# Performance work log

Measured on AMD Instinct MI355X. Metric: run time of the kernel, lower is better.

## Reference

```python
import jax, jax.numpy as jnp
import numpy as np

BITS = 4
GROUP = 128
MAXQ = 2 ** BITS - 1  # 15 for asymmetric 4-bit


def round_ste(x):
    # straight-through rounding: round in fwd, identity in bwd
    return x + jax.lax.stop_gradient(jnp.round(x) - x)


def quant_weight(weight, v, min_scale, max_scale):
    """Groupwise asymmetric fake-quant (quantize + dequantize) of weight.

    weight: [O, I], v: [O, I] learnable rounding offsets,
    min_scale/max_scale: [O*I/GROUP] learnable min/max scales in [-1, 0].
    """
    O, I = weight.shape
    w = weight.reshape(-1, GROUP)          # [G, GROUP]
    vv = v.reshape(-1, GROUP)              # [G, GROUP]
    wmin_t = jnp.minimum(w.min(axis=1), 0.0)  # [G]
    wmax_t = jnp.maximum(w.max(axis=1), 0.0)  # [G]
    # forward clamps min/max scale into [-1, 0] before use
    wmin = wmin_t * (jnp.clip(min_scale, -1.0, 0.0) + 1.0)
    wmax = wmax_t * (jnp.clip(max_scale, -1.0, 0.0) + 1.0)
    degenerate = (wmin == 0.0) & (wmax == 0.0)
    wmin = jnp.where(degenerate, -1.0, wmin)
    wmax = jnp.where(degenerate, 1.0, wmax)
    # scale stored at fp16 precision (scale_dtype), then used in fp32 math
    scale = ((wmax - wmin) / MAXQ).astype(jnp.float16).astype(weight.dtype)  # [G]
    zp = round_ste(-wmin / scale)                                            # [G]
    int_w = round_ste(w / scale[:, None] + vv)                               # [G, GROUP]
    q = jnp.clip(int_w + zp[:, None], 0.0, float(MAXQ))
    wq = scale[:, None] * (q - zp[:, None])
    return wq.reshape(O, I)


def setup_inputs() -> dict:
    key = jax.random.key(0)
    k_x, k_w, k_b, k_v = jax.random.split(key, 4)
    O, I = 4096, 4096
    B, S = 2, 2048
    x = jax.random.normal(k_x, (B, S, I), dtype=jnp.float32)
    weight = jax.random.normal(k_w, (O, I), dtype=jnp.float32) * 0.02
    bias = jax.random.normal(k_b, (O,), dtype=jnp.float32) * 0.02
    value = jax.random.normal(k_v, (O, I), dtype=jnp.float32) * 0.1
    n_groups = O * I // GROUP
    min_scale = jnp.zeros((n_groups,), dtype=jnp.float32)
    max_scale = jnp.zeros((n_groups,), dtype=jnp.float32)
    return {"x": x, "weight": weight, "bias": bias, "value": value,
            "min_scale": min_scale, "max_scale": max_scale}


def reference(x, weight, bias, value, min_scale, max_scale):
    wq = quant_weight(weight, value, min_scale, max_scale)  # [O, I]
    # F.linear(x, weight_q, bias): x @ wq.T + bias
    return jnp.einsum('bsi,oi->bso', x, wq) + bias
```

## Files before the change

### kernel.cpp

```cpp
#include <hip/hip_runtime.h>
#include <hip/hip_bf16.h>
#include <hip/hip_fp16.h>
#include <stdint.h>

#define M_DIM 4096
#define N_DIM 4096
#define K_DIM 4096
#define GROUPSZ 128
#define MAXQ 15.0f

#define BM 256
#define BN 256
#define BK 64
#define T_TILES (K_DIM / BK)

typedef __attribute__((ext_vector_type(8))) short short8;
typedef __attribute__((ext_vector_type(4))) float f32x4;

__global__ __launch_bounds__(256) void quant_kernel(
    const float* __restrict__ weight, const float* __restrict__ value,
    const float* __restrict__ min_scale, const float* __restrict__ max_scale,
    __hip_bfloat16* __restrict__ wq)
{
    const int tid  = threadIdx.x;
    const int wave = tid >> 6;
    const int lane = tid & 63;
    const long g    = (long)blockIdx.x * 4 + wave;
    const long base = g * GROUPSZ + lane * 2;

    const float2 w = *(const float2*)(weight + base);
    const float2 v = *(const float2*)(value  + base);

    float mn = fminf(w.x, w.y);
    float mx = fmaxf(w.x, w.y);
#pragma unroll
    for (int off = 32; off >= 1; off >>= 1) {
        mn = fminf(mn, __shfl_xor(mn, off, 64));
        mx = fmaxf(mx, __shfl_xor(mx, off, 64));
    }
    mn = fminf(mn, 0.0f);
    mx = fmaxf(mx, 0.0f);

    const float ms = fminf(fmaxf(min_scale[g], -1.0f), 0.0f) + 1.0f;
    const float xs = fminf(fmaxf(max_scale[g], -1.0f), 0.0f) + 1.0f;
    float wmin = mn * ms;
    float wmax = mx * xs;
    if (wmin == 0.0f && wmax == 0.0f) { wmin = -1.0f; wmax = 1.0f; }

    const float scale = (float)(_Float16)((wmax - wmin) / MAXQ);
    const float zp    = rintf(-wmin / scale);

    const float q0 = fminf(fmaxf(rintf(w.x / scale + v.x) + zp, 0.0f), MAXQ);
    const float q1 = fminf(fmaxf(rintf(w.y / scale + v.y) + zp, 0.0f), MAXQ);
    const float o0 = scale * (q0 - zp);
    const float o1 = scale * (q1 - zp);

    __hip_bfloat162 o;
    o.x = __float2bfloat16(o0);
    o.y = __float2bfloat16(o1);
    *(__hip_bfloat162*)(wq + base) = o;
}

__global__ __launch_bounds__(256) void cast_kernel(
    const float* __restrict__ x, __hip_bfloat16* __restrict__ xb)
{
    const long i = ((long)blockIdx.x * 256 + threadIdx.x) * 8;
    const float4 a = *(const float4*)(x + i);
    const float4 b = *(const float4*)(x + i + 4);
    union { short8 s; __hip_bfloat16 h[8]; } u;
    u.h[0] = __float2bfloat16(a.x);
    u.h[1] = __float2bfloat16(a.y);
    u.h[2] = __float2bfloat16(a.z);
    u.h[3] = __float2bfloat16(a.w);
    u.h[4] = __float2bfloat16(b.x);
    u.h[5] = __float2bfloat16(b.y);
    u.h[6] = __float2bfloat16(b.z);
    u.h[7] = __float2bfloat16(b.w);
    *(short8*)(xb + i) = u.s;
}

__global__ __launch_bounds__(512, 2) void gemm_kernel(
    const __hip_bfloat16* __restrict__ A,
    const __hip_bfloat16* __restrict__ B,
    const float* __restrict__ bias,
    float* __restrict__ C)
{
    __shared__ __align__(16) char lds[131072];

    const int tid  = threadIdx.x;
    const int lane = tid & 63;
    const int wv   = tid >> 6;
    const int wm   = wv >> 2;
    const int wn   = wv & 3;

    const int bid = blockIdx.x;
    const int swz = (bid & 7) * (gridDim.x >> 3) + (bid >> 3);
    const int brow = (swz >> 4) * BM;
    const int bcol = (swz & 15) * BN;

    const int stg_r = tid >> 3;
    const int cc    = ((tid & 7) ^ (stg_r & 7)) * 8;

#define STAGE(XP, rowbase, h, tau, ldsbase)                                         \
    { _Pragma("unroll")                                                             \
      for (int inst = 0; inst < 2; ++inst) {                                        \
        const __hip_bfloat16* g = (XP) +                                            \
            (size_t)((rowbase) + (h) * 128 + inst * 64 + stg_r) * K_DIM +           \
            (tau) * 64 + cc;                                                        \
        __builtin_amdgcn_global_load_lds(                                           \
            (const __attribute__((address_space(1))) void*)g,                       \
            (__attribute__((address_space(3))) void*)(lds + (ldsbase) +             \
                (h) * 16384 + inst * 8192 + (wv << 10)),                            \
            16, 0, 0);                                                              \
      } }

    const int ro = lane & 15;
    const int hi = lane >> 4;
    const int slot0 = ((0 + hi) ^ (ro & 7)) << 4;
    const int slot1 = ((4 + hi) ^ (ro & 7)) << 4;
    const int rbA = (wm * 128 + ro) * 128;
    const int rbB = (wn * 64  + ro) * 128;

    f32x4 acc[8][4] = {};

    STAGE(B, bcol, 0, 0, 65536);
    STAGE(B, bcol, 1, 0, 65536);
    STAGE(A, brow, 0, 0, 0);
    STAGE(A, brow, 1, 0, 0);
    STAGE(B, bcol, 0, 1, 65536 + 32768);
    STAGE(B, bcol, 1, 1, 65536 + 32768);
    STAGE(A, brow, 0, 1, 32768);
    asm volatile("s_waitcnt vmcnt(6)" ::: "memory");
    __builtin_amdgcn_s_barrier();

#define MFMA_PAIR(M0)                                                               \
    { _Pragma("unroll")                                                             \
      for (int n = 0; n < 4; ++n) {                                                 \
        acc[M0][n]     = __builtin_amdgcn_mfma_f32_16x16x32_bf16(af[M0][0],   b0[n][0], acc[M0][n],     0, 0, 0); \
        acc[M0 + 1][n] = __builtin_amdgcn_mfma_f32_16x16x32_bf16(af[M0+1][0], b0[n][0], acc[M0 + 1][n], 0, 0, 0); \
        acc[M0][n]     = __builtin_amdgcn_mfma_f32_16x16x32_bf16(af[M0][1],   b0[n][1], acc[M0][n],     0, 0, 0); \
        acc[M0 + 1][n] = __builtin_amdgcn_mfma_f32_16x16x32_bf16(af[M0+1][1], b0[n][1], acc[M0 + 1][n], 0, 0, 0); \
      } }

    for (int t = 0; t < T_TILES; ++t) {
        const int c = t & 1;
        const char* bA = lds + c * 32768 + rbA;
        const char* bB = lds + 65536 + c * 32768 + rbB;

        short8 b0[4][2];
        short8 af[8][2];

#pragma unroll
        for (int n = 0; n < 4; ++n) {
            b0[n][0] = *(const short8*)(bB + n * 2048 + slot0);
            b0[n][1] = *(const short8*)(bB + n * 2048 + slot1);
        }
#pragma unroll
        for (int m = 0; m < 4; ++m) {
            af[m][0] = *(const short8*)(bA + m * 2048 + slot0);
            af[m][1] = *(const short8*)(bA + m * 2048 + slot1);
        }
        if (t + 1 < T_TILES) { STAGE(A, brow, 1, t + 1, (c ^ 1) * 32768); }
        __builtin_amdgcn_s_barrier();
        asm volatile("s_waitcnt lgkmcnt(0)" ::: "memory");
        __builtin_amdgcn_s_setprio(1);
        MFMA_PAIR(0);
        __builtin_amdgcn_s_setprio(0);
        __builtin_amdgcn_s_barrier();

#pragma unroll
        for (int m = 4; m < 6; ++m) {
            af[m][0] = *(const short8*)(bA + m * 2048 + slot0);
            af[m][1] = *(const short8*)(bA + m * 2048 + slot1);
        }
        if (t + 2 < T_TILES) { STAGE(B, bcol, 0, t + 2, 65536 + c * 32768); }
        __builtin_amdgcn_s_barrier();
        asm volatile("s_waitcnt lgkmcnt(0)" ::: "memory");
        __builtin_amdgcn_s_setprio(1);
        MFMA_PAIR(2);
        __builtin_amdgcn_s_setprio(0);
        __builtin_amdgcn_s_barrier();

#pragma unroll
        for (int m = 6; m < 8; ++m) {
            af[m][0] = *(const short8*)(bA + m * 2048 + slot0);
            af[m][1] = *(const short8*)(bA + m * 2048 + slot1);
        }
        if (t + 2 < T_TILES) { STAGE(B, bcol, 1, t + 2, 65536 + c * 32768); }
        __builtin_amdgcn_s_barrier();
        asm volatile("s_waitcnt lgkmcnt(0)" ::: "memory");
        __builtin_amdgcn_s_setprio(1);
        MFMA_PAIR(4);
        __builtin_amdgcn_s_setprio(0);
        __builtin_amdgcn_s_barrier();

        if (t + 2 < T_TILES) { STAGE(A, brow, 0, t + 2, c * 32768); }
        if (t < T_TILES - 2) { asm volatile("s_waitcnt vmcnt(6)" ::: "memory"); }
        else                 { asm volatile("s_waitcnt vmcnt(0)" ::: "memory"); }
        __builtin_amdgcn_s_barrier();
        __builtin_amdgcn_s_setprio(1);
        MFMA_PAIR(6);
        __builtin_amdgcn_s_setprio(0);
        __builtin_amdgcn_s_barrier();
    }

    const int col   = lane & 15;
    const int rbase = hi * 4;
    float bv[4];
#pragma unroll
    for (int n = 0; n < 4; ++n)
        bv[n] = bias[bcol + wn * 64 + n * 16 + col];

#pragma unroll
    for (int m = 0; m < 8; ++m) {
        const int mrow = brow + wm * 128 + m * 16 + rbase;
#pragma unroll
        for (int r = 0; r < 4; ++r) {
            float* crow = C + (size_t)(mrow + r) * N_DIM + bcol + wn * 64 + col;
#pragma unroll
            for (int n = 0; n < 4; ++n)
                crow[n * 16] = acc[m][n][r] + bv[n];
        }
    }
#undef STAGE
#undef MFMA_PAIR
}

extern "C" void kernel_launch(void* const* d_in, const int* in_sizes, int n_in,
                              void* d_out, int out_size, void* d_ws, size_t ws_size,
                              hipStream_t stream) {
    const float* x         = (const float*)d_in[0];
    const float* weight    = (const float*)d_in[1];
    const float* bias      = (const float*)d_in[2];
    const float* value     = (const float*)d_in[3];
    const float* min_scale = (const float*)d_in[4];
    const float* max_scale = (const float*)d_in[5];
    float* out = (float*)d_out;

    __hip_bfloat16* xb  = (__hip_bfloat16*)d_ws;
    __hip_bfloat16* wqb = xb + (size_t)M_DIM * K_DIM;

    quant_kernel<<<(N_DIM * K_DIM / GROUPSZ) / 4, 256, 0, stream>>>(
        weight, value, min_scale, max_scale, wqb);
    cast_kernel<<<(M_DIM * K_DIM) / (256 * 8), 256, 0, stream>>>(x, xb);
    gemm_kernel<<<(M_DIM / BM) * (N_DIM / BN), 512, 0, stream>>>(xb, wqb, bias, out);
}
```

Baseline: 172.1 us.

## Rework GEMM A-tile prefetch schedule and shrink A fragment registers

```diff
diff --git a/kernel.cpp b/kernel.cpp
--- a/kernel.cpp
+++ b/kernel.cpp
@@ -129,77 +129,76 @@
     STAGE(A, brow, 1, 0, 0);
     STAGE(B, bcol, 0, 1, 65536 + 32768);
     STAGE(B, bcol, 1, 1, 65536 + 32768);
-    STAGE(A, brow, 0, 1, 32768);
-    asm volatile("s_waitcnt vmcnt(6)" ::: "memory");
+    asm volatile("s_waitcnt vmcnt(4)" ::: "memory");
     __builtin_amdgcn_s_barrier();
 
-#define MFMA_PAIR(M0)                                                               \
+#define MFMA16(M0, XA0, XA1)                                                        \
     { _Pragma("unroll")                                                             \
       for (int n = 0; n < 4; ++n) {                                                 \
-        acc[M0][n]     = __builtin_amdgcn_mfma_f32_16x16x32_bf16(af[M0][0],   b0[n][0], acc[M0][n],     0, 0, 0); \
-        acc[M0 + 1][n] = __builtin_amdgcn_mfma_f32_16x16x32_bf16(af[M0+1][0], b0[n][0], acc[M0 + 1][n], 0, 0, 0); \
-        acc[M0][n]     = __builtin_amdgcn_mfma_f32_16x16x32_bf16(af[M0][1],   b0[n][1], acc[M0][n],     0, 0, 0); \
-        acc[M0 + 1][n] = __builtin_amdgcn_mfma_f32_16x16x32_bf16(af[M0+1][1], b0[n][1], acc[M0 + 1][n], 0, 0, 0); \
+        acc[M0][n]     = __builtin_amdgcn_mfma_f32_16x16x32_bf16((XA0)[0], bfr[n][0], acc[M0][n],     0, 0, 0); \
+        acc[M0 + 1][n] = __builtin_amdgcn_mfma_f32_16x16x32_bf16((XA1)[0], bfr[n][0], acc[M0 + 1][n], 0, 0, 0); \
+      }                                                                             \
+      _Pragma("unroll")                                                             \
+      for (int n = 0; n < 4; ++n) {                                                 \
+        acc[M0][n]     = __builtin_amdgcn_mfma_f32_16x16x32_bf16((XA0)[1], bfr[n][1], acc[M0][n],     0, 0, 0); \
+        acc[M0 + 1][n] = __builtin_amdgcn_mfma_f32_16x16x32_bf16((XA1)[1], bfr[n][1], acc[M0 + 1][n], 0, 0, 0); \
       } }
+
+#define LD_A(dst, m)                                                                \
+    dst[0] = *(const short8*)(bA + (m) * 2048 + slot0);                             \
+    dst[1] = *(const short8*)(bA + (m) * 2048 + slot1);
 
     for (int t = 0; t < T_TILES; ++t) {
         const int c = t & 1;
         const char* bA = lds + c * 32768 + rbA;
         const char* bB = lds + 65536 + c * 32768 + rbB;
 
-        short8 b0[4][2];
-        short8 af[8][2];
+        short8 bfr[4][2];
+        short8 x0[2], x1[2];
 
 #pragma unroll
         for (int n = 0; n < 4; ++n) {
-            b0[n][0] = *(const short8*)(bB + n * 2048 + slot0);
-            b0[n][1] = *(const short8*)(bB + n * 2048 + slot1);
+            bfr[n][0] = *(const short8*)(bB + n * 2048 + slot0);
+            bfr[n][1] = *(const short8*)(bB + n * 2048 + slot1);
         }
-#pragma unroll
-        for (int m = 0; m < 4; ++m) {
-            af[m][0] = *(const short8*)(bA + m * 2048 + slot0);
-            af[m][1] = *(const short8*)(bA + m * 2048 + slot1);
+        LD_A(x0, 0); LD_A(x1, 1);
+        if (t + 1 < T_TILES) {
+            STAGE(A, brow, 0, t + 1, (c ^ 1) * 32768);
+            STAGE(A, brow, 1, t + 1, (c ^ 1) * 32768);
         }
-        if (t + 1 < T_TILES) { STAGE(A, brow, 1, t + 1, (c ^ 1) * 32768); }
-        __builtin_amdgcn_s_barrier();
-        asm volatile("s_waitcnt lgkmcnt(0)" ::: "memory");
-        __builtin_amdgcn_s_setprio(1);
-        MFMA_PAIR(0);
-        __builtin_amdgcn_s_setprio(0);
-        __builtin_amdgcn_s_barrier();
-
-#pragma unroll
-        for (int m = 4; m < 6; ++m) {
-            af[m][0] = *(const short8*)(bA + m * 2048 + slot0);
-            af[m][1] = *(const short8*)(bA + m * 2048 + slot1);
-        }
+        asm volatile("s_waitcnt lgkmcnt(8)" ::: "memory");
+        __builtin_amdgcn_s_barrier();
+        asm volatile("s_waitcnt lgkmcnt(0)" ::: "memory");
+        __builtin_amdgcn_s_setprio(1);
+        MFMA16(0, x0, x1);
+        __builtin_amdgcn_s_setprio(0);
+        __builtin_amdgcn_s_barrier();
+
+        LD_A(x0, 2); LD_A(x1, 3);
         if (t + 2 < T_TILES) { STAGE(B, bcol, 0, t + 2, 65536 + c * 32768); }
         __builtin_amdgcn_s_barrier();
         asm volatile("s_waitcnt lgkmcnt(0)" ::: "memory");
         __builtin_amdgcn_s_setprio(1);
-        MFMA_PAIR(2);
-        __builtin_amdgcn_s_setprio(0);
-        __builtin_amdgcn_s_barrier();
-
-#pragma unroll
-        for (int m = 6; m < 8; ++m) {
-            af[m][0] = *(const short8*)(bA + m * 2048 + slot0);
-            af[m][1] = *(const short8*)(bA + m * 2048 + slot1);
-        }
+        MFMA16(2, x0, x1);
+        __builtin_amdgcn_s_setprio(0);
+        __builtin_amdgcn_s_barrier();
+
+        LD_A(x0, 4); LD_A(x1, 5);
         if (t + 2 < T_TILES) { STAGE(B, bcol, 1, t + 2, 65536 + c * 32768); }
         __builtin_amdgcn_s_barrier();
         asm volatile("s_waitcnt lgkmcnt(0)" ::: "memory");
         __builtin_amdgcn_s_setprio(1);
-        MFMA_PAIR(4);
-        __builtin_amdgcn_s_setprio(0);
-        __builtin_amdgcn_s_barrier();
-
-        if (t + 2 < T_TILES) { STAGE(A, brow, 0, t + 2, c * 32768); }
-        if (t < T_TILES - 2) { asm volatile("s_waitcnt vmcnt(6)" ::: "memory"); }
+        MFMA16(4, x0, x1);
+        __builtin_amdgcn_s_setprio(0);
+        __builtin_amdgcn_s_barrier();
+
+        LD_A(x0, 6); LD_A(x1, 7);
+        if (t < T_TILES - 2) { asm volatile("s_waitcnt vmcnt(4)" ::: "memory"); }
         else                 { asm volatile("s_waitcnt vmcnt(0)" ::: "memory"); }
         __builtin_amdgcn_s_barrier();
-        __builtin_amdgcn_s_setprio(1);
-        MFMA_PAIR(6);
+        asm volatile("s_waitcnt lgkmcnt(0)" ::: "memory");
+        __builtin_amdgcn_s_setprio(1);
+        MFMA16(6, x0, x1);
         __builtin_amdgcn_s_setprio(0);
         __builtin_amdgcn_s_barrier();
     }
@@ -223,7 +222,8 @@
         }
     }
 #undef STAGE
-#undef MFMA_PAIR
+#undef MFMA16
+#undef LD_A
 }
 
 extern "C" void kernel_launch(void* const* d_in, const int* in_sizes, int n_in,
```

Result: no change. 172.3 us (+0.1%).
